# Kernel tuning notes

Measured on AMD Instinct MI355X. Metric: run time of the kernel, lower is better.

## Reference

```python
import jax, jax.numpy as jnp
import numpy as np

N = 50000          # nodes
E = 800000         # edges (avg degree 16)
F = 128            # in_dim = num_hidden*heads = pred_dim
H = 4              # attention heads per layer
D = 32             # num_hidden (per-head dim)
R = 11             # rel_num
L = 2              # num_layers
SCALE = float(1.0 / np.sqrt(D))


def setup_inputs() -> dict:
    key = jax.random.key(0)
    ks = jax.random.split(key, 16)
    inputs = jax.random.normal(ks[0], (N, F), jnp.float32)
    edge_types = jax.random.randint(ks[1], (E,), 0, R)
    src = jax.random.randint(ks[2], (E,), 0, N)
    dst = jax.random.randint(ks[3], (E,), 0, N)
    centrality = jax.random.uniform(ks[4], (N,), jnp.float32)
    rel_emb = jax.random.normal(ks[5], (R, F), jnp.float32) * 0.1
    # stacked per-layer projection weights (both layers have F -> H*D = F)
    Wq = jax.random.normal(ks[6], (L, F, H * D), jnp.float32) * 0.05
    Wk = jax.random.normal(ks[7], (L, F, H * D), jnp.float32) * 0.05
    Wv = jax.random.normal(ks[8], (L, F, H * D), jnp.float32) * 0.05
    We = jax.random.normal(ks[9], (L, F, H * D), jnp.float32) * 0.05
    bq = jnp.zeros((L, H * D), jnp.float32)
    bk = jnp.zeros((L, H * D), jnp.float32)
    bv = jnp.zeros((L, H * D), jnp.float32)
    be = jnp.zeros((L, H * D), jnp.float32)
    W_out = jax.random.normal(ks[10], (H * D, 1), jnp.float32) * 0.05
    b_out = jnp.zeros((1,), jnp.float32)
    gamma = jnp.ones((1,), jnp.float32)
    beta = jnp.zeros((1,), jnp.float32)
    return {"inputs": inputs, "edge_types": edge_types, "src": src, "dst": dst,
            "centrality": centrality, "rel_emb": rel_emb,
            "Wq": Wq, "bq": bq, "Wk": Wk, "bk": bk, "Wv": Wv, "bv": bv,
            "We": We, "be": be, "W_out": W_out, "b_out": b_out,
            "gamma": gamma, "beta": beta}


def _segment_softmax(score, dst, n):
    # score: [E, H]; softmax over incoming edges of each dst node
    m = jax.ops.segment_max(score, dst, num_segments=n)          # [N, H]
    ex = jnp.exp(score - m[dst])                                  # [E, H]
    s = jax.ops.segment_sum(ex, dst, num_segments=n)              # [N, H]
    return ex / (s[dst] + 1e-9)


def reference(inputs, edge_types, src, dst, centrality, rel_emb,
              Wq, bq, Wk, bk, Wv, bv, We, be, W_out, b_out, gamma, beta):
    h = inputs                                   # [N, F]
    ef = rel_emb[edge_types]                     # [E, pred_dim] relational edge embedding
    for l in range(L):
        q = (h @ Wq[l] + bq[l]).reshape(N, H, D)
        k = (h @ Wk[l] + bk[l]).reshape(N, H, D)
        v = (h @ Wv[l] + bv[l]).reshape(N, H, D)
        e = (ef @ We[l] + be[l]).reshape(E, H, D)
        # edge_mode="add": edge features added to keys/values on each edge
        ke = k[src] + e                           # [E, H, D]
        score = jnp.sum(q[dst] * ke, axis=-1) * SCALE   # [E, H]
        attn = _segment_softmax(score, dst, N)          # [E, H]
        msg = attn[:, :, None] * (v[src] + e)           # [E, H, D]
        agg = jax.ops.segment_sum(msg, dst, num_segments=N)  # [N, H, D]
        # identity residual (in_dim == H*D) + ELU activation
        h = jax.nn.elu(agg.reshape(N, H * D) + h)
    logits = h @ W_out + b_out                    # [N, 1]
    logits = jax.nn.relu((centrality * gamma + beta)[:, None] * logits)
    return logits
```

## Files before the change

### kernel.cpp

```cpp
#include <hip/hip_runtime.h>
#include <hip/hip_bf16.h>
#include <math.h>

#define SCALE_C 0.17677669529663687f
#define CAPP 64

typedef short bf16x8 __attribute__((ext_vector_type(8)));
typedef float f32x4 __attribute__((ext_vector_type(4)));
typedef _Float16 h16x2 __attribute__((ext_vector_type(2)));
typedef unsigned u32x4 __attribute__((ext_vector_type(4)));

__device__ __forceinline__ h16x2 bch2(unsigned u) { return __builtin_bit_cast(h16x2, u); }

__device__ __forceinline__ uint4 nt_load16(const void* p) {
  u32x4 v = __builtin_nontemporal_load((const u32x4*)p);
  return __builtin_bit_cast(uint4, v);
}


__global__ __launch_bounds__(256) void prep_scatter_k(
    const float* __restrict__ Wq, const float* __restrict__ Wk, const float* __restrict__ Wv,
    __hip_bfloat16* __restrict__ wf,
    const float* __restrict__ rel_emb, const float* __restrict__ We, const float* __restrict__ be,
    _Float16* __restrict__ re, int R, int reb,
    const int* __restrict__ dst, const int* __restrict__ src, const int* __restrict__ etype,
    int E, int* __restrict__ cnt, int* __restrict__ bins) {
  int b = blockIdx.x;
  if (b < 48) {
    int tid = b * 256 + threadIdx.x;
    int lane = tid & 63;
    int frag = tid >> 6;
    int ks = frag & 3;
    int ct = (frag >> 2) & 7;
    int mat = frag >> 5;
    int l = mat / 3, m = mat % 3;
    const float* W = ((m == 0) ? Wq : (m == 1) ? Wk : Wv) + (size_t)l * 128 * 128;
    int nn = ct * 16 + (lane & 15);
    int k0 = ks * 32 + (lane >> 4) * 8;
    __hip_bfloat16 tmp[8];
    #pragma unroll
    for (int j = 0; j < 8; ++j) tmp[j] = __float2bfloat16(W[(size_t)(k0 + j) * 128 + nn]);
    *(uint4*)&wf[(size_t)frag * 64 * 8 + (size_t)lane * 8] = *(const uint4*)tmp;
  } else if (b < 48 + reb) {
    int idx = (b - 48) * 256 + threadIdx.x;
    int tot = 2 * R * 128;
    if (idx >= tot) return;
    int c = idx & 127;
    int r = (idx >> 7) % R;
    int l = idx / (R * 128);
    const float* W = We + (size_t)l * 128 * 128;
    float acc = be[l * 128 + c];
    #pragma unroll 4
    for (int kk = 0; kk < 128; ++kk) acc += rel_emb[r * 128 + kk] * W[kk * 128 + c];
    re[idx] = (_Float16)acc;
  } else {
    int e = (b - 48 - reb) * 256 + threadIdx.x;
    if (e < E) {
      int d = dst[e];
      int pos = atomicAdd(&cnt[d], 1);
      if (pos < CAPP) bins[(d << 6) + pos] = src[e] | (etype[e] << 20);
    }
  }
}


__device__ __forceinline__ void qkv_body(
    const float* __restrict__ Xf, const __hip_bfloat16* __restrict__ Xb,
    const __hip_bfloat16* __restrict__ wf,
    const float* __restrict__ bq, const float* __restrict__ bk, const float* __restrict__ bv,
    _Float16* __restrict__ qo, _Float16* __restrict__ kvo, int n, int bid) {
  __shared__ __attribute__((aligned(16))) __hip_bfloat16 xs[32][136];
  __shared__ __attribute__((aligned(16))) _Float16 ot[3][32][136];
  int tid = threadIdx.x;
  int wid = tid >> 6;
  int lane = tid & 63;
  int row0 = bid * 32;
  if (row0 >= n) return;

  for (int idx = tid; idx < 512; idx += 192) {
    int row = idx >> 4, g = idx & 15;
    union { uint4 u; __hip_bfloat16 h[8]; } P;
    P.u = make_uint4(0, 0, 0, 0);
    if (row0 + row < n) {
      if (Xb) {
        P.u = *(const uint4*)(Xb + (size_t)(row0 + row) * 128 + g * 8);
      } else {
        const float* xr = Xf + (size_t)(row0 + row) * 128 + g * 8;
        float4 x0 = *(const float4*)xr;
        float4 x1 = *(const float4*)(xr + 4);
        P.h[0] = __float2bfloat16(x0.x); P.h[1] = __float2bfloat16(x0.y);
        P.h[2] = __float2bfloat16(x0.z); P.h[3] = __float2bfloat16(x0.w);
        P.h[4] = __float2bfloat16(x1.x); P.h[5] = __float2bfloat16(x1.y);
        P.h[6] = __float2bfloat16(x1.z); P.h[7] = __float2bfloat16(x1.w);
      }
    }
    *(uint4*)&xs[row][g * 8] = P.u;
  }
  __syncthreads();

  int cl = lane & 15;
  int quad = lane >> 4;

  bf16x8 afrag[2][4];
  #pragma unroll
  for (int s = 0; s < 2; ++s)
    #pragma unroll
    for (int ks = 0; ks < 4; ++ks)
      afrag[s][ks] = *(const bf16x8*)&xs[s * 16 + cl][quad * 8 + ks * 32];

  const uint4* wfu = (const uint4*)wf;
  const float* bias = (wid == 0) ? bq : (wid == 1) ? bk : bv;
  float scl = (wid == 0) ? SCALE_C : 1.0f;

  #pragma unroll
  for (int ct = 0; ct < 8; ++ct) {
    f32x4 a0 = {0.f, 0.f, 0.f, 0.f}, a1 = {0.f, 0.f, 0.f, 0.f};
    #pragma unroll
    for (int ks = 0; ks < 4; ++ks) {
      uint4 braw = wfu[((size_t)(wid * 8 + ct) * 4 + ks) * 64 + lane];
      bf16x8 bfr = __builtin_bit_cast(bf16x8, braw);
      a0 = __builtin_amdgcn_mfma_f32_16x16x32_bf16(afrag[0][ks], bfr, a0, 0, 0, 0);
      a1 = __builtin_amdgcn_mfma_f32_16x16x32_bf16(afrag[1][ks], bfr, a1, 0, 0, 0);
    }
    int c = ct * 16 + cl;
    float bb = bias[c];
    #pragma unroll
    for (int r = 0; r < 4; ++r) {
      ot[wid][quad * 4 + r][c]      = (_Float16)((a0[r] + bb) * scl);
      ot[wid][16 + quad * 4 + r][c] = (_Float16)((a1[r] + bb) * scl);
    }
  }

  if (wid == 0) {
    #pragma unroll
    for (int it = 0; it < 8; ++it) {
      int idx = it * 64 + lane;
      int row = idx >> 4, g = idx & 15;
      if (row0 + row < n)
        *(uint4*)&qo[(size_t)(row0 + row) * 128 + g * 8] = *(const uint4*)&ot[0][row][g * 8];
    }
  } else {
    int off = (wid == 1) ? 0 : 128;
    #pragma unroll
    for (int it = 0; it < 8; ++it) {
      int idx = it * 64 + lane;
      int row = idx >> 4, g = idx & 15;
      if (row0 + row < n)
        *(uint4*)&kvo[(size_t)(row0 + row) * 256 + off + g * 8] = *(const uint4*)&ot[wid][row][g * 8];
    }
  }
}

__global__ __launch_bounds__(192) void qkv1_k(
    const float* __restrict__ Xf, const __hip_bfloat16* __restrict__ wf,
    const float* __restrict__ bq, const float* __restrict__ bk, const float* __restrict__ bv,
    _Float16* __restrict__ qo, _Float16* __restrict__ kvo, int n) {
  qkv_body(Xf, nullptr, wf, bq, bk, bv, qo, kvo, n, blockIdx.x);
}

__global__ __launch_bounds__(192) void qkv2_k(
    const __hip_bfloat16* __restrict__ Xb, const __hip_bfloat16* __restrict__ wf,
    const float* __restrict__ bq, const float* __restrict__ bk, const float* __restrict__ bv,
    _Float16* __restrict__ qo, _Float16* __restrict__ kvo, int n) {
  qkv_body(nullptr, Xb, wf, bq, bk, bv, qo, kvo, n, blockIdx.x);
}


__global__ __launch_bounds__(256) void edge_k(
    const _Float16* __restrict__ qb, const _Float16* __restrict__ kv,
    const _Float16* __restrict__ re,
    const int* __restrict__ bins, const int* __restrict__ cnt,
    const float* __restrict__ h_in_f, const __hip_bfloat16* __restrict__ h_in_b,
    __hip_bfloat16* __restrict__ h_out_b,
    const float* __restrict__ Wout, const float* __restrict__ bout,
    const float* __restrict__ cent, const float* __restrict__ gamma,
    const float* __restrict__ beta, float* __restrict__ outp, int n) {
  int node = blockIdx.x * 4 + (threadIdx.x >> 6);
  if (node >= n) return;
  int lane = threadIdx.x & 63;
  int j = lane & 15;
  int quarter = lane >> 4;
  int deg = cnt[node];
  deg = deg < CAPP ? deg : CAPP;
  uint nm1 = (uint)(n - 1);

  int pkrow = (lane < deg) ? __builtin_nontemporal_load(bins + (node << 6) + lane) : 0;

  uint4 qraw = nt_load16((const uint4*)(qb + ((size_t)node << 7)) + j);

  float4 h0, h1;
  if (h_in_b) {
    uint4 hraw = nt_load16((const uint4*)(h_in_b + ((size_t)node << 7)) + j);
    h0.x = __uint_as_float(hraw.x << 16); h0.y = __uint_as_float(hraw.x & 0xffff0000u);
    h0.z = __uint_as_float(hraw.y << 16); h0.w = __uint_as_float(hraw.y & 0xffff0000u);
    h1.x = __uint_as_float(hraw.z << 16); h1.y = __uint_as_float(hraw.z & 0xffff0000u);
    h1.z = __uint_as_float(hraw.w << 16); h1.w = __uint_as_float(hraw.w & 0xffff0000u);
  } else {
    const float4* hrow = (const float4*)h_in_f + ((uint)node * 32u + (uint)(j * 2));
    uint4 t0 = nt_load16(hrow);
    uint4 t1 = nt_load16(hrow + 1);
    h0.x = __uint_as_float(t0.x); h0.y = __uint_as_float(t0.y);
    h0.z = __uint_as_float(t0.z); h0.w = __uint_as_float(t0.w);
    h1.x = __uint_as_float(t1.x); h1.y = __uint_as_float(t1.y);
    h1.z = __uint_as_float(t1.z); h1.w = __uint_as_float(t1.w);
  }

  h16x2 q01 = bch2(qraw.x), q23 = bch2(qraw.y), q45 = bch2(qraw.z), q67 = bch2(qraw.w);
  float qa0 = (float)q01.x, qa1 = (float)q01.y;
  float qa2 = (float)q23.x, qa3 = (float)q23.y;
  float qa4 = (float)q45.x, qa5 = (float)q45.y;
  float qa6 = (float)q67.x, qa7 = (float)q67.y;

  float ssum = 0.f;
  float acc0 = 0.f, acc1 = 0.f, acc2 = 0.f, acc3 = 0.f;
  float acc4 = 0.f, acc5 = 0.f, acc6 = 0.f, acc7 = 0.f;

  int nit = (deg + 3) >> 2;
  nit = (nit + 1) & ~1;

  const uint4* kvb  = (const uint4*)kv + (uint)j;
  const uint4* rebp = (const uint4*)re + (uint)j;

  auto loadstage = [&](int pk, uint4& rk, uint4& rv, uint4& rr) {
    uint s = (uint)pk & 0xFFFFFu; s = s < nm1 ? s : nm1;
    uint t = (uint)pk >> 20;
    const uint4* kp = kvb + s * 32u;
    rk = kp[0];
    rv = kp[16];
    rr = rebp[t * 16u];
  };
  auto accum = [&](uint4 rk, uint4 rv, uint4 rr, int eidx) {
    h16x2 r01 = bch2(rr.x), r23 = bch2(rr.y), r45 = bch2(rr.z), r67 = bch2(rr.w);
    h16x2 kr01 = bch2(rk.x) + r01;
    h16x2 kr23 = bch2(rk.y) + r23;
    h16x2 kr45 = bch2(rk.z) + r45;
    h16x2 kr67 = bch2(rk.w) + r67;
    h16x2 vr01 = bch2(rv.x) + r01;
    h16x2 vr23 = bch2(rv.y) + r23;
    h16x2 vr45 = bch2(rv.z) + r45;
    h16x2 vr67 = bch2(rv.w) + r67;
    float pA = qa0 * (float)kr01.x;
    pA += qa1 * (float)kr01.y;
    pA += qa2 * (float)kr23.x;
    pA += qa3 * (float)kr23.y;
    float pB = qa4 * (float)kr45.x;
    pB += qa5 * (float)kr45.y;
    pB += qa6 * (float)kr67.x;
    pB += qa7 * (float)kr67.y;
    float p = pA + pB;
    p += __shfl_xor(p, 1);
    p += __shfl_xor(p, 2);
    float w = (eidx < deg) ? __expf(p) : 0.f;
    ssum += w;
    acc0 += w * (float)vr01.x;
    acc1 += w * (float)vr01.y;
    acc2 += w * (float)vr23.x;
    acc3 += w * (float)vr23.y;
    acc4 += w * (float)vr45.x;
    acc5 += w * (float)vr45.y;
    acc6 += w * (float)vr67.x;
    acc7 += w * (float)vr67.y;
  };

  uint4 a0, a1, ar, b0, b1, br;
  loadstage(__shfl(pkrow, quarter), a0, a1, ar);
  loadstage(__shfl(pkrow, 4 + quarter), b0, b1, br);

  for (int i = 0; i < nit; i += 2) {
    bool more = (i + 2) < nit;
    int pkA2 = 0, pkB2 = 0;
    if (more) {
      pkA2 = __shfl(pkrow, (4 * i + 8 + quarter) & 63);
      pkB2 = __shfl(pkrow, (4 * i + 12 + quarter) & 63);
    }
    accum(a0, a1, ar, 4 * i + quarter);
    if (more) loadstage(pkA2, a0, a1, ar);
    accum(b0, b1, br, 4 * i + 4 + quarter);
    if (more) loadstage(pkB2, b0, b1, br);
  }

  ssum += __shfl_xor(ssum, 16); ssum += __shfl_xor(ssum, 32);
  acc0 += __shfl_xor(acc0, 16); acc0 += __shfl_xor(acc0, 32);
  acc1 += __shfl_xor(acc1, 16); acc1 += __shfl_xor(acc1, 32);
  acc2 += __shfl_xor(acc2, 16); acc2 += __shfl_xor(acc2, 32);
  acc3 += __shfl_xor(acc3, 16); acc3 += __shfl_xor(acc3, 32);
  acc4 += __shfl_xor(acc4, 16); acc4 += __shfl_xor(acc4, 32);
  acc5 += __shfl_xor(acc5, 16); acc5 += __shfl_xor(acc5, 32);
  acc6 += __shfl_xor(acc6, 16); acc6 += __shfl_xor(acc6, 32);
  acc7 += __shfl_xor(acc7, 16); acc7 += __shfl_xor(acc7, 32);
  if (quarter != 0) return;

  float inv = __builtin_amdgcn_rcpf(ssum + 1e-9f);
  float x0 = acc0 * inv + h0.x;
  float x1 = acc1 * inv + h0.y;
  float x2 = acc2 * inv + h0.z;
  float x3 = acc3 * inv + h0.w;
  float x4 = acc4 * inv + h1.x;
  float x5 = acc5 * inv + h1.y;
  float x6 = acc6 * inv + h1.z;
  float x7 = acc7 * inv + h1.w;
  x0 = x0 > 0.f ? x0 : __expf(x0) - 1.f;
  x1 = x1 > 0.f ? x1 : __expf(x1) - 1.f;
  x2 = x2 > 0.f ? x2 : __expf(x2) - 1.f;
  x3 = x3 > 0.f ? x3 : __expf(x3) - 1.f;
  x4 = x4 > 0.f ? x4 : __expf(x4) - 1.f;
  x5 = x5 > 0.f ? x5 : __expf(x5) - 1.f;
  x6 = x6 > 0.f ? x6 : __expf(x6) - 1.f;
  x7 = x7 > 0.f ? x7 : __expf(x7) - 1.f;
  if (outp == nullptr) {
    union { uint4 u; __hip_bfloat16 hh[8]; } P;
    P.hh[0] = __float2bfloat16(x0); P.hh[1] = __float2bfloat16(x1);
    P.hh[2] = __float2bfloat16(x2); P.hh[3] = __float2bfloat16(x3);
    P.hh[4] = __float2bfloat16(x4); P.hh[5] = __float2bfloat16(x5);
    P.hh[6] = __float2bfloat16(x6); P.hh[7] = __float2bfloat16(x7);
    *((uint4*)(h_out_b + ((size_t)node << 7)) + j) = P.u;
  } else {
    const float4* wrow = (const float4*)Wout + (uint)(j * 2);
    float4 w0 = wrow[0], w1 = wrow[1];
    float pp = x0 * w0.x + x1 * w0.y + x2 * w0.z + x3 * w0.w
             + x4 * w1.x + x5 * w1.y + x6 * w1.z + x7 * w1.w;
    pp += __shfl_xor(pp, 1);
    pp += __shfl_xor(pp, 2);
    pp += __shfl_xor(pp, 4);
    pp += __shfl_xor(pp, 8);
    if (lane == 0) {
      float lg = pp + bout[0];
      lg *= (cent[node] * gamma[0] + beta[0]);
      outp[node] = fmaxf(lg, 0.f);
    }
  }
}


extern "C" void kernel_launch(void* const* d_in, const int* in_sizes, int n_in,
                              void* d_out, int out_size, void* d_ws, size_t ws_size,
                              hipStream_t stream) {
  const float* inputs  = (const float*)d_in[0];
  const int*   etype   = (const int*)d_in[1];
  const int*   src     = (const int*)d_in[2];
  const int*   dst     = (const int*)d_in[3];
  const float* cent    = (const float*)d_in[4];
  const float* rel_emb = (const float*)d_in[5];
  const float* Wq      = (const float*)d_in[6];
  const float* bq      = (const float*)d_in[7];
  const float* Wk      = (const float*)d_in[8];
  const float* bk      = (const float*)d_in[9];
  const float* Wv      = (const float*)d_in[10];
  const float* bv      = (const float*)d_in[11];
  const float* We      = (const float*)d_in[12];
  const float* be      = (const float*)d_in[13];
  const float* Wout    = (const float*)d_in[14];
  const float* bout    = (const float*)d_in[15];
  const float* gamma   = (const float*)d_in[16];
  const float* beta    = (const float*)d_in[17];
  float* out = (float*)d_out;

  const int N = in_sizes[0] / 128;
  const int E = in_sizes[1];
  const int R = in_sizes[5] / 128;

  _Float16* re = (_Float16*)d_ws;
  __hip_bfloat16* hb = (__hip_bfloat16*)(re + 2 * (size_t)R * 128);
  _Float16* qb = (_Float16*)(hb + (size_t)N * 128);
  _Float16* kv = qb + (size_t)N * 128;
  __hip_bfloat16* wf = (__hip_bfloat16*)(kv + (size_t)N * 256);
  int* cnt  = (int*)(wf + 6 * 16384);
  int* bins = cnt + N;

  hipMemsetAsync(cnt, 0, (size_t)N * sizeof(int), stream);

  int reb = (2 * R * 128 + 255) / 256;
  int SB  = (E + 255) / 256;
  prep_scatter_k<<<48 + reb + SB, 256, 0, stream>>>(Wq, Wk, Wv, wf, rel_emb, We, be, re, R, reb,
                                                    dst, src, etype, E, cnt, bins);

  int QB = (N + 31) / 32;
  int eb = (N + 3) / 4;
  qkv1_k<<<QB, 192, 0, stream>>>(inputs, wf, bq, bk, bv, qb, kv, N);
  edge_k<<<eb, 256, 0, stream>>>(qb, kv, re, bins, cnt,
                                 inputs, nullptr, hb,
                                 Wout, bout, cent, gamma, beta, nullptr, N);
  qkv2_k<<<QB, 192, 0, stream>>>(hb, wf + (size_t)3 * 16384,
                                 bq + 128, bk + 128, bv + 128, qb, kv, N);
  edge_k<<<eb, 256, 0, stream>>>(qb, kv, re + (size_t)R * 128, bins, cnt,
                                 nullptr, hb, nullptr,
                                 Wout, bout, cent, gamma, beta, out, N);
}
```

Before: 301.3 us.

## Fuse edge binning into first QKV kernel and zero counts in prep kernel

Removes the separate memset by zeroing node counts inside the prep kernel, and moves the atomic edge-binning scatter out of the prep kernel into extra blocks of the first QKV projection kernel, so the scatter runs concurrently with the layer-1 GEMM. The edge kernel now reads bin entries directly from global memory per iteration instead of loading a whole row into a register and broadcasting it with shuffles. Indices are clamped to 63 so reads stay inside the bin row. The tradeoff is more global loads per iteration in the edge kernel and contention between scatter blocks and GEMM blocks.

```diff
diff --git a/kernel.cpp b/kernel.cpp
--- a/kernel.cpp
+++ b/kernel.cpp
@@ -18,13 +18,12 @@
 }
 
 
-__global__ __launch_bounds__(256) void prep_scatter_k(
+__global__ __launch_bounds__(256) void prep0_k(
     const float* __restrict__ Wq, const float* __restrict__ Wk, const float* __restrict__ Wv,
     __hip_bfloat16* __restrict__ wf,
     const float* __restrict__ rel_emb, const float* __restrict__ We, const float* __restrict__ be,
     _Float16* __restrict__ re, int R, int reb,
-    const int* __restrict__ dst, const int* __restrict__ src, const int* __restrict__ etype,
-    int E, int* __restrict__ cnt, int* __restrict__ bins) {
+    int* __restrict__ cnt, int N) {
   int b = blockIdx.x;
   if (b < 48) {
     int tid = b * 256 + threadIdx.x;
@@ -54,12 +53,8 @@
     for (int kk = 0; kk < 128; ++kk) acc += rel_emb[r * 128 + kk] * W[kk * 128 + c];
     re[idx] = (_Float16)acc;
   } else {
-    int e = (b - 48 - reb) * 256 + threadIdx.x;
-    if (e < E) {
-      int d = dst[e];
-      int pos = atomicAdd(&cnt[d], 1);
-      if (pos < CAPP) bins[(d << 6) + pos] = src[e] | (etype[e] << 20);
-    }
+    int idx = (b - 48 - reb) * 256 + threadIdx.x;
+    if (idx < N) cnt[idx] = 0;
   }
 }
 
@@ -151,11 +146,23 @@
   }
 }
 
-__global__ __launch_bounds__(192) void qkv1_k(
+
+__global__ __launch_bounds__(192) void qkv1s_k(
     const float* __restrict__ Xf, const __hip_bfloat16* __restrict__ wf,
     const float* __restrict__ bq, const float* __restrict__ bk, const float* __restrict__ bv,
-    _Float16* __restrict__ qo, _Float16* __restrict__ kvo, int n) {
-  qkv_body(Xf, nullptr, wf, bq, bk, bv, qo, kvo, n, blockIdx.x);
+    _Float16* __restrict__ qo, _Float16* __restrict__ kvo, int n, int QB,
+    const int* __restrict__ dst, const int* __restrict__ src, const int* __restrict__ etype,
+    int E, int* __restrict__ cnt, int* __restrict__ bins) {
+  if ((int)blockIdx.x < QB) {
+    qkv_body(Xf, nullptr, wf, bq, bk, bv, qo, kvo, n, blockIdx.x);
+  } else {
+    int e = (blockIdx.x - QB) * 192 + threadIdx.x;
+    if (e < E) {
+      int d = dst[e];
+      int pos = atomicAdd(&cnt[d], 1);
+      if (pos < CAPP) bins[(d << 6) + pos] = src[e] | (etype[e] << 20);
+    }
+  }
 }
 
 __global__ __launch_bounds__(192) void qkv2_k(
@@ -180,11 +187,10 @@
   int lane = threadIdx.x & 63;
   int j = lane & 15;
   int quarter = lane >> 4;
+  int rs = node << 6;
   int deg = cnt[node];
   deg = deg < CAPP ? deg : CAPP;
   uint nm1 = (uint)(n - 1);
-
-  int pkrow = (lane < deg) ? __builtin_nontemporal_load(bins + (node << 6) + lane) : 0;
 
   uint4 qraw = nt_load16((const uint4*)(qb + ((size_t)node << 7)) + j);
 
@@ -263,16 +269,15 @@
   };
 
   uint4 a0, a1, ar, b0, b1, br;
-  loadstage(__shfl(pkrow, quarter), a0, a1, ar);
-  loadstage(__shfl(pkrow, 4 + quarter), b0, b1, br);
+  loadstage(bins[rs + quarter], a0, a1, ar);
+  loadstage(bins[rs + quarter + 4], b0, b1, br);
 
   for (int i = 0; i < nit; i += 2) {
     bool more = (i + 2) < nit;
-    int pkA2 = 0, pkB2 = 0;
-    if (more) {
-      pkA2 = __shfl(pkrow, (4 * i + 8 + quarter) & 63);
-      pkB2 = __shfl(pkrow, (4 * i + 12 + quarter) & 63);
-    }
+    int e2a = 4 * i + 8 + quarter;  e2a = e2a < 63 ? e2a : 63;
+    int e2b = 4 * i + 12 + quarter; e2b = e2b < 63 ? e2b : 63;
+    int pkA2 = bins[rs + e2a];
+    int pkB2 = bins[rs + e2b];
     accum(a0, a1, ar, 4 * i + quarter);
     if (more) loadstage(pkA2, a0, a1, ar);
     accum(b0, b1, br, 4 * i + 4 + quarter);
@@ -367,16 +372,16 @@
   int* cnt  = (int*)(wf + 6 * 16384);
   int* bins = cnt + N;
 
-  hipMemsetAsync(cnt, 0, (size_t)N * sizeof(int), stream);
-
   int reb = (2 * R * 128 + 255) / 256;
-  int SB  = (E + 255) / 256;
-  prep_scatter_k<<<48 + reb + SB, 256, 0, stream>>>(Wq, Wk, Wv, wf, rel_emb, We, be, re, R, reb,
-                                                    dst, src, etype, E, cnt, bins);
+  int CB  = (N + 255) / 256;
+  prep0_k<<<48 + reb + CB, 256, 0, stream>>>(Wq, Wk, Wv, wf, rel_emb, We, be, re, R, reb,
+                                             cnt, N);
 
   int QB = (N + 31) / 32;
+  int SB = (E + 191) / 192;
   int eb = (N + 3) / 4;
-  qkv1_k<<<QB, 192, 0, stream>>>(inputs, wf, bq, bk, bv, qb, kv, N);
+  qkv1s_k<<<QB + SB, 192, 0, stream>>>(inputs, wf, bq, bk, bv, qb, kv, N, QB,
+                                       dst, src, etype, E, cnt, bins);
   edge_k<<<eb, 256, 0, stream>>>(qb, kv, re, bins, cnt,
                                  inputs, nullptr, hb,
                                  Wout, bout, cent, gamma, beta, nullptr, N);
```

Result: slower. 320.0 us (+6.2%).

## Split QKV projection into per-matrix blocks with direct-to-register A loads

Applied to the files above, without the earlier changes.

The QKV projection kernel now launches three times as many blocks. Each block computes one of Q, K or V for 32 rows with two waves, instead of one block of three waves covering all three matrices. The A fragments are loaded straight from global memory into registers, with the fp32-to-bf16 conversion done in registers, which removes the shared-memory staging and its barrier. This raises parallelism and cuts LDS use, but each input row is now read three times from global memory (once per matrix block).

```diff
diff --git a/kernel.cpp b/kernel.cpp
--- a/kernel.cpp
+++ b/kernel.cpp
@@ -67,102 +67,83 @@
 __device__ __forceinline__ void qkv_body(
     const float* __restrict__ Xf, const __hip_bfloat16* __restrict__ Xb,
     const __hip_bfloat16* __restrict__ wf,
-    const float* __restrict__ bq, const float* __restrict__ bk, const float* __restrict__ bv,
-    _Float16* __restrict__ qo, _Float16* __restrict__ kvo, int n, int bid) {
-  __shared__ __attribute__((aligned(16))) __hip_bfloat16 xs[32][136];
-  __shared__ __attribute__((aligned(16))) _Float16 ot[3][32][136];
+    const float* __restrict__ bias, float scl,
+    _Float16* __restrict__ op, int ostride, int mat, int n, int rowblk) {
+  __shared__ __attribute__((aligned(16))) _Float16 ot[32][136];
   int tid = threadIdx.x;
   int wid = tid >> 6;
   int lane = tid & 63;
-  int row0 = bid * 32;
+  int row0 = rowblk * 32;
   if (row0 >= n) return;
-
-  for (int idx = tid; idx < 512; idx += 192) {
-    int row = idx >> 4, g = idx & 15;
-    union { uint4 u; __hip_bfloat16 h[8]; } P;
-    P.u = make_uint4(0, 0, 0, 0);
-    if (row0 + row < n) {
-      if (Xb) {
-        P.u = *(const uint4*)(Xb + (size_t)(row0 + row) * 128 + g * 8);
-      } else {
-        const float* xr = Xf + (size_t)(row0 + row) * 128 + g * 8;
-        float4 x0 = *(const float4*)xr;
-        float4 x1 = *(const float4*)(xr + 4);
-        P.h[0] = __float2bfloat16(x0.x); P.h[1] = __float2bfloat16(x0.y);
-        P.h[2] = __float2bfloat16(x0.z); P.h[3] = __float2bfloat16(x0.w);
-        P.h[4] = __float2bfloat16(x1.x); P.h[5] = __float2bfloat16(x1.y);
-        P.h[6] = __float2bfloat16(x1.z); P.h[7] = __float2bfloat16(x1.w);
-      }
-    }
-    *(uint4*)&xs[row][g * 8] = P.u;
-  }
-  __syncthreads();
-
   int cl = lane & 15;
   int quad = lane >> 4;
 
-  bf16x8 afrag[2][4];
-  #pragma unroll
-  for (int s = 0; s < 2; ++s)
-    #pragma unroll
-    for (int ks = 0; ks < 4; ++ks)
-      afrag[s][ks] = *(const bf16x8*)&xs[s * 16 + cl][quad * 8 + ks * 32];
+  bf16x8 afrag[4];
+  int arow = row0 + wid * 16 + cl;
+  bool av = arow < n;
+  if (Xb) {
+    const __hip_bfloat16* xr = Xb + (size_t)arow * 128 + quad * 8;
+    #pragma unroll
+    for (int ks = 0; ks < 4; ++ks) {
+      uint4 raw = av ? *(const uint4*)(xr + ks * 32) : make_uint4(0, 0, 0, 0);
+      afrag[ks] = __builtin_bit_cast(bf16x8, raw);
+    }
+  } else {
+    const float* xr = Xf + (size_t)arow * 128 + quad * 8;
+    #pragma unroll
+    for (int ks = 0; ks < 4; ++ks) {
+      float4 x0 = av ? *(const float4*)(xr + ks * 32)     : make_float4(0.f, 0.f, 0.f, 0.f);
+      float4 x1 = av ? *(const float4*)(xr + ks * 32 + 4) : make_float4(0.f, 0.f, 0.f, 0.f);
+      union { bf16x8 v; __hip_bfloat16 h[8]; } fu;
+      fu.h[0] = __float2bfloat16(x0.x); fu.h[1] = __float2bfloat16(x0.y);
+      fu.h[2] = __float2bfloat16(x0.z); fu.h[3] = __float2bfloat16(x0.w);
+      fu.h[4] = __float2bfloat16(x1.x); fu.h[5] = __float2bfloat16(x1.y);
+      fu.h[6] = __float2bfloat16(x1.z); fu.h[7] = __float2bfloat16(x1.w);
+      afrag[ks] = fu.v;
+    }
+  }
 
   const uint4* wfu = (const uint4*)wf;
-  const float* bias = (wid == 0) ? bq : (wid == 1) ? bk : bv;
-  float scl = (wid == 0) ? SCALE_C : 1.0f;
 
   #pragma unroll
   for (int ct = 0; ct < 8; ++ct) {
-    f32x4 a0 = {0.f, 0.f, 0.f, 0.f}, a1 = {0.f, 0.f, 0.f, 0.f};
+    f32x4 a = {0.f, 0.f, 0.f, 0.f};
     #pragma unroll
     for (int ks = 0; ks < 4; ++ks) {
-      uint4 braw = wfu[((size_t)(wid * 8 + ct) * 4 + ks) * 64 + lane];
+      uint4 braw = wfu[((size_t)(mat * 8 + ct) * 4 + ks) * 64 + lane];
       bf16x8 bfr = __builtin_bit_cast(bf16x8, braw);
-      a0 = __builtin_amdgcn_mfma_f32_16x16x32_bf16(afrag[0][ks], bfr, a0, 0, 0, 0);
-      a1 = __builtin_amdgcn_mfma_f32_16x16x32_bf16(afrag[1][ks], bfr, a1, 0, 0, 0);
+      a = __builtin_amdgcn_mfma_f32_16x16x32_bf16(afrag[ks], bfr, a, 0, 0, 0);
     }
     int c = ct * 16 + cl;
     float bb = bias[c];
     #pragma unroll
-    for (int r = 0; r < 4; ++r) {
-      ot[wid][quad * 4 + r][c]      = (_Float16)((a0[r] + bb) * scl);
-      ot[wid][16 + quad * 4 + r][c] = (_Float16)((a1[r] + bb) * scl);
-    }
-  }
-
-  if (wid == 0) {
-    #pragma unroll
-    for (int it = 0; it < 8; ++it) {
-      int idx = it * 64 + lane;
-      int row = idx >> 4, g = idx & 15;
-      if (row0 + row < n)
-        *(uint4*)&qo[(size_t)(row0 + row) * 128 + g * 8] = *(const uint4*)&ot[0][row][g * 8];
-    }
-  } else {
-    int off = (wid == 1) ? 0 : 128;
-    #pragma unroll
-    for (int it = 0; it < 8; ++it) {
-      int idx = it * 64 + lane;
-      int row = idx >> 4, g = idx & 15;
-      if (row0 + row < n)
-        *(uint4*)&kvo[(size_t)(row0 + row) * 256 + off + g * 8] = *(const uint4*)&ot[wid][row][g * 8];
-    }
-  }
-}
-
-__global__ __launch_bounds__(192) void qkv1_k(
-    const float* __restrict__ Xf, const __hip_bfloat16* __restrict__ wf,
+    for (int r = 0; r < 4; ++r)
+      ot[wid * 16 + quad * 4 + r][c] = (_Float16)((a[r] + bb) * scl);
+  }
+
+  #pragma unroll
+  for (int it = 0; it < 4; ++it) {
+    int idx = it * 64 + lane;
+    int row = wid * 16 + (idx >> 4);
+    int g = idx & 15;
+    if (row0 + row < n)
+      *(uint4*)&op[(size_t)(row0 + row) * ostride + g * 8] = *(const uint4*)&ot[row][g * 8];
+  }
+}
+
+__global__ __launch_bounds__(128) void qkv_k(
+    const float* __restrict__ Xf, const __hip_bfloat16* __restrict__ Xb,
+    const __hip_bfloat16* __restrict__ wf,
     const float* __restrict__ bq, const float* __restrict__ bk, const float* __restrict__ bv,
-    _Float16* __restrict__ qo, _Float16* __restrict__ kvo, int n) {
-  qkv_body(Xf, nullptr, wf, bq, bk, bv, qo, kvo, n, blockIdx.x);
-}
-
-__global__ __launch_bounds__(192) void qkv2_k(
-    const __hip_bfloat16* __restrict__ Xb, const __hip_bfloat16* __restrict__ wf,
-    const float* __restrict__ bq, const float* __restrict__ bk, const float* __restrict__ bv,
-    _Float16* __restrict__ qo, _Float16* __restrict__ kvo, int n) {
-  qkv_body(nullptr, Xb, wf, bq, bk, bv, qo, kvo, n, blockIdx.x);
+    _Float16* __restrict__ qo, _Float16* __restrict__ kvo, int n, int QB) {
+  int bid = blockIdx.x;
+  int mat = bid / QB;
+  int rowblk = bid - mat * QB;
+  const float* bias = (mat == 0) ? bq : (mat == 1) ? bk : bv;
+  float scl = (mat == 0) ? SCALE_C : 1.0f;
+  _Float16* op = (mat == 0) ? qo : (kvo + ((mat == 1) ? 0 : 128));
+  int ostride = (mat == 0) ? 128 : 256;
+  qkv_body(Xf, Xb, wf, bias, scl, op, ostride, mat, n, rowblk);
 }
 
 
@@ -376,12 +357,12 @@
 
   int QB = (N + 31) / 32;
   int eb = (N + 3) / 4;
-  qkv1_k<<<QB, 192, 0, stream>>>(inputs, wf, bq, bk, bv, qb, kv, N);
+  qkv_k<<<3 * QB, 128, 0, stream>>>(inputs, nullptr, wf, bq, bk, bv, qb, kv, N, QB);
   edge_k<<<eb, 256, 0, stream>>>(qb, kv, re, bins, cnt,
                                  inputs, nullptr, hb,
                                  Wout, bout, cent, gamma, beta, nullptr, N);
-  qkv2_k<<<QB, 192, 0, stream>>>(hb, wf + (size_t)3 * 16384,
-                                 bq + 128, bk + 128, bv + 128, qb, kv, N);
+  qkv_k<<<3 * QB, 128, 0, stream>>>(nullptr, hb, wf + (size_t)3 * 16384,
+                                    bq + 128, bk + 128, bv + 128, qb, kv, N, QB);
   edge_k<<<eb, 256, 0, stream>>>(qb, kv, re + (size_t)R * 128, bins, cnt,
                                  nullptr, hb, nullptr,
                                  Wout, bout, cent, gamma, beta, out, N);
```

New measurement: 323.8 us. +7.5%, slower.
